# Kernel tuning notes

Measured on AMD Instinct MI355X. Metric: run time of the kernel, lower is better.

Reference implementation:

```python
import itertools
import jax, jax.numpy as jnp
import numpy as np

EPS = 1.1920928955078125e-07  # torch.finfo(float32).eps, used by torchmetrics SI-SNR


def setup_inputs() -> dict:
    key = jax.random.key(0)
    k1, k2 = jax.random.split(key)
    B, S, T = 32, 2, 256000
    preds = jax.random.normal(k1, (B, S, T), dtype=jnp.float32)
    targets = jax.random.normal(k2, (B, S, T), dtype=jnp.float32)
    return {"preds": preds, "targets": targets}


def _pit_sisnr_loss(preds, targets):
    # preds, targets: [B, S, T]
    B, S, T = preds.shape
    # torchmetrics SI-SNR zero-means both signals along time
    p = preds - jnp.mean(preds, axis=-1, keepdims=True)
    t = targets - jnp.mean(targets, axis=-1, keepdims=True)
    # pairwise statistics: pred i vs target j
    dot = jnp.einsum('bit,bjt->bij', p, t)          # <p_i, t_j>        [B,S,S]
    tt = jnp.sum(t * t, axis=-1)                    # ||t_j||^2          [B,S]
    pp = jnp.sum(p * p, axis=-1)                    # ||p_i||^2          [B,S]
    alpha = dot / (tt[:, None, :] + EPS)            # projection scale   [B,S,S]
    s_target = alpha * alpha * tt[:, None, :]       # ||alpha * t||^2
    # ||p - alpha*t||^2 expanded (no [B,S,S,T] intermediate)
    noise = pp[:, :, None] - 2.0 * alpha * dot + s_target
    sisnr = 10.0 * jnp.log10((s_target + EPS) / (noise + EPS))  # [B,S,S]
    # PIT: max over all speaker permutations of the mean matched SI-SNR
    perms = np.array(list(itertools.permutations(range(S))))    # [P,S]
    rows = np.arange(S)[None, :]                                # [1,S]
    perm_scores = sisnr[:, rows, perms].mean(axis=-1)           # [B,P]
    best = perm_scores.max(axis=-1)                             # [B]
    return -jnp.mean(best)


def reference(preds, targets):
    return _pit_sisnr_loss(preds, targets)
```

## Files before the change

### kernel.cpp

```cpp
#include <hip/hip_runtime.h>

#define EPS 1.1920928955078125e-07f


__global__ __launch_bounds__(256) void pit_partials(
    const float* __restrict__ preds, const float* __restrict__ targets,
    float* __restrict__ ws, int T, int chunks_per_b)
{
    const int b = blockIdx.x / chunks_per_b;
    const int c = blockIdx.x % chunks_per_b;
    const int T4 = T >> 2;
    const int chunk = T4 / chunks_per_b;

    const float4* p0 = (const float4*)(preds   + (size_t)(b * 2 + 0) * T);
    const float4* p1 = (const float4*)(preds   + (size_t)(b * 2 + 1) * T);
    const float4* t0 = (const float4*)(targets + (size_t)(b * 2 + 0) * T);
    const float4* t1 = (const float4*)(targets + (size_t)(b * 2 + 1) * T);

    float acc[12];
#pragma unroll
    for (int k = 0; k < 12; ++k) acc[k] = 0.f;

    const int beg = c * chunk;
    const int end = beg + chunk;
    for (int i = beg + (int)threadIdx.x; i < end; i += 256) {
        float4 a0 = p0[i];
        float4 a1 = p1[i];
        float4 b0 = t0[i];
        float4 b1 = t1[i];
#pragma unroll
        for (int e = 0; e < 4; ++e) {
            float u0 = (&a0.x)[e], u1 = (&a1.x)[e];
            float v0 = (&b0.x)[e], v1 = (&b1.x)[e];
            acc[0]  += u0;       acc[1]  += u1;
            acc[2]  += v0;       acc[3]  += v1;
            acc[4]  += u0 * u0;  acc[5]  += u1 * u1;
            acc[6]  += v0 * v0;  acc[7]  += v1 * v1;
            acc[8]  += u0 * v0;  acc[9]  += u0 * v1;
            acc[10] += u1 * v0;  acc[11] += u1 * v1;
        }
    }

    const int lane = threadIdx.x & 63;
    const int wave = threadIdx.x >> 6;
#pragma unroll
    for (int k = 0; k < 12; ++k) {
        float v = acc[k];
        for (int off = 32; off > 0; off >>= 1) v += __shfl_down(v, off);
        acc[k] = v;
    }

    __shared__ float lds[4][12];
    if (lane == 0) {
#pragma unroll
        for (int k = 0; k < 12; ++k) lds[wave][k] = acc[k];
    }
    __syncthreads();

    if (threadIdx.x < 12) {
        float v = lds[0][threadIdx.x] + lds[1][threadIdx.x]
                + lds[2][threadIdx.x] + lds[3][threadIdx.x];
        atomicAdd(&ws[(size_t)b * 12 + threadIdx.x], v);
    }
}

__global__ __launch_bounds__(64) void pit_final(
    const float* __restrict__ ws, float* __restrict__ out, int B, int T)
{
    const int b = threadIdx.x;
    float best = 0.f;
    if (b < B) {
        const float* w = ws + (size_t)b * 12;
        const float invT = 1.0f / (float)T;
        float pp0 = w[4] - w[0] * w[0] * invT;
        float pp1 = w[5] - w[1] * w[1] * invT;
        float tt0 = w[6] - w[2] * w[2] * invT;
        float tt1 = w[7] - w[3] * w[3] * invT;
        float d00 = w[8]  - w[0] * w[2] * invT;
        float d01 = w[9]  - w[0] * w[3] * invT;
        float d10 = w[10] - w[1] * w[2] * invT;
        float d11 = w[11] - w[1] * w[3] * invT;

        auto sisnr = [](float dot, float pp, float tt) -> float {
            float alpha = dot / (tt + EPS);
            float st    = alpha * alpha * tt;
            float noise = pp - 2.0f * alpha * dot + st;
            return 10.0f * log10f((st + EPS) / (noise + EPS));
        };
        float s00 = sisnr(d00, pp0, tt0);
        float s01 = sisnr(d01, pp0, tt1);
        float s10 = sisnr(d10, pp1, tt0);
        float s11 = sisnr(d11, pp1, tt1);

        float perm0 = 0.5f * (s00 + s11);
        float perm1 = 0.5f * (s01 + s10);
        best = fmaxf(perm0, perm1);
    }
    for (int off = 32; off > 0; off >>= 1) best += __shfl_down(best, off);
    if (threadIdx.x == 0) out[0] = -best / (float)B;
}

extern "C" void kernel_launch(void* const* d_in, const int* in_sizes, int n_in,
                              void* d_out, int out_size, void* d_ws, size_t ws_size,
                              hipStream_t stream)
{
    const float* preds   = (const float*)d_in[0];
    const float* targets = (const float*)d_in[1];
    float* out = (float*)d_out;
    float* ws  = (float*)d_ws;

    const int B = 32;
    const int T = 256000;
    const int chunks_per_b = 25;

    hipMemsetAsync(ws, 0, (size_t)B * 12 * sizeof(float), stream);

    pit_partials<<<dim3(B * chunks_per_b), dim3(256), 0, stream>>>(preds, targets, ws, T, chunks_per_b);
    pit_final<<<dim3(1), dim3(64), 0, stream>>>(ws, out, B, T);
}
```

Measured before the change: 148.5 us.

## Double chunk count, fully unroll with compile-time sizes, replace atomics with per-block partials

Doubles the per-batch chunk count to 50, giving 1600 blocks instead of 800 to fill more CUs. Sizes become compile-time constants so the streaming loop of 5 iterations is fully unrolled, and launch bounds request 4 blocks per CU. Global atomics and the memset launch are replaced by per-block partial writes that the final kernel reduces over 50 chunks per batch. This removes one launch and the atomic contention, but shifts more serial reduction work into a single-block final kernel.

Result: no change. 146.8 us (-1.1%).

```diff
diff --git a/kernel.cpp b/kernel.cpp
--- a/kernel.cpp
+++ b/kernel.cpp
@@ -2,28 +2,35 @@
 
 #define EPS 1.1920928955078125e-07f
 
+#define BB 32
+#define TT 256000
+#define CHUNKS 50
+#define T4 (TT / 4)
+#define CHUNK (T4 / CHUNKS)
+#define ITERS (CHUNK / 256)
+#define NBLK (BB * CHUNKS)
 
-__global__ __launch_bounds__(256) void pit_partials(
+
+__global__ __launch_bounds__(256, 4) void pit_partials(
     const float* __restrict__ preds, const float* __restrict__ targets,
-    float* __restrict__ ws, int T, int chunks_per_b)
+    float* __restrict__ ws)
 {
-    const int b = blockIdx.x / chunks_per_b;
-    const int c = blockIdx.x % chunks_per_b;
-    const int T4 = T >> 2;
-    const int chunk = T4 / chunks_per_b;
+    const int b = blockIdx.x / CHUNKS;
+    const int c = blockIdx.x % CHUNKS;
 
-    const float4* p0 = (const float4*)(preds   + (size_t)(b * 2 + 0) * T);
-    const float4* p1 = (const float4*)(preds   + (size_t)(b * 2 + 1) * T);
-    const float4* t0 = (const float4*)(targets + (size_t)(b * 2 + 0) * T);
-    const float4* t1 = (const float4*)(targets + (size_t)(b * 2 + 1) * T);
+    const float4* p0 = (const float4*)(preds   + (size_t)(b * 2 + 0) * TT);
+    const float4* p1 = (const float4*)(preds   + (size_t)(b * 2 + 1) * TT);
+    const float4* t0 = (const float4*)(targets + (size_t)(b * 2 + 0) * TT);
+    const float4* t1 = (const float4*)(targets + (size_t)(b * 2 + 1) * TT);
 
     float acc[12];
 #pragma unroll
     for (int k = 0; k < 12; ++k) acc[k] = 0.f;
 
-    const int beg = c * chunk;
-    const int end = beg + chunk;
-    for (int i = beg + (int)threadIdx.x; i < end; i += 256) {
+    const int base = c * CHUNK + (int)threadIdx.x;
+#pragma unroll
+    for (int it = 0; it < ITERS; ++it) {
+        const int i = base + it * 256;
         float4 a0 = p0[i];
         float4 a1 = p1[i];
         float4 b0 = t0[i];
@@ -60,18 +67,30 @@
     if (threadIdx.x < 12) {
         float v = lds[0][threadIdx.x] + lds[1][threadIdx.x]
                 + lds[2][threadIdx.x] + lds[3][threadIdx.x];
-        atomicAdd(&ws[(size_t)b * 12 + threadIdx.x], v);
+        ws[(size_t)blockIdx.x * 12 + threadIdx.x] = v;
     }
 }
 
-__global__ __launch_bounds__(64) void pit_final(
-    const float* __restrict__ ws, float* __restrict__ out, int B, int T)
+__global__ __launch_bounds__(256) void pit_final(
+    const float* __restrict__ ws, float* __restrict__ out)
 {
-    const int b = threadIdx.x;
-    float best = 0.f;
-    if (b < B) {
-        const float* w = ws + (size_t)b * 12;
-        const float invT = 1.0f / (float)T;
+    __shared__ float sums[BB * 12];
+    __shared__ float bests[BB];
+
+    for (int s = threadIdx.x; s < BB * 12; s += 256) {
+        const int b = s / 12;
+        const int k = s % 12;
+        float v = 0.f;
+        const float* base = ws + (size_t)(b * CHUNKS) * 12 + k;
+#pragma unroll 10
+        for (int c = 0; c < CHUNKS; ++c) v += base[(size_t)c * 12];
+        sums[s] = v;
+    }
+    __syncthreads();
+
+    if (threadIdx.x < BB) {
+        const float* w = sums + threadIdx.x * 12;
+        const float invT = 1.0f / (float)TT;
         float pp0 = w[4] - w[0] * w[0] * invT;
         float pp1 = w[5] - w[1] * w[1] * invT;
         float tt0 = w[6] - w[2] * w[2] * invT;
@@ -94,10 +113,16 @@
 
         float perm0 = 0.5f * (s00 + s11);
         float perm1 = 0.5f * (s01 + s10);
-        best = fmaxf(perm0, perm1);
+        bests[threadIdx.x] = fmaxf(perm0, perm1);
     }
-    for (int off = 32; off > 0; off >>= 1) best += __shfl_down(best, off);
-    if (threadIdx.x == 0) out[0] = -best / (float)B;
+    __syncthreads();
+
+    if (threadIdx.x == 0) {
+        float acc = 0.f;
+#pragma unroll
+        for (int b = 0; b < BB; ++b) acc += bests[b];
+        out[0] = -acc / (float)BB;
+    }
 }
 
 extern "C" void kernel_launch(void* const* d_in, const int* in_sizes, int n_in,
@@ -109,12 +134,6 @@
     float* out = (float*)d_out;
     float* ws  = (float*)d_ws;
 
-    const int B = 32;
-    const int T = 256000;
-    const int chunks_per_b = 25;
-
-    hipMemsetAsync(ws, 0, (size_t)B * 12 * sizeof(float), stream);
-
-    pit_partials<<<dim3(B * chunks_per_b), dim3(256), 0, stream>>>(preds, targets, ws, T, chunks_per_b);
-    pit_final<<<dim3(1), dim3(64), 0, stream>>>(ws, out, B, T);
+    pit_partials<<<dim3(NBLK), dim3(256), 0, stream>>>(preds, targets, ws);
+    pit_final<<<dim3(1), dim3(256), 0, stream>>>(ws, out);
 }
```
